# Performance work log

Hardware: AMD Instinct MI355X
Metric: run time of the kernel (lower is better)

## Reference

```python
import jax, jax.numpy as jnp
import numpy as np


def setup_inputs() -> dict:
    key = jax.random.key(0)
    k1, k2, k3 = jax.random.split(key, 3)
    B, D, T, DEPTH = 16384, 512, 64, 6
    x = jax.random.normal(k1, (B, D), dtype=jnp.float32)
    # per-tree learned params, stacked over the tree axis (num_trees)
    feature_selectors = jax.random.normal(k2, (T, DEPTH, D), dtype=jnp.float32)
    thresholds = jnp.zeros((T, DEPTH), dtype=jnp.float32)
    leaf_weights = jax.random.normal(k3, (T, 2 ** DEPTH, 1), dtype=jnp.float32)
    return {"x": x, "feature_selectors": feature_selectors,
            "thresholds": thresholds, "leaf_weights": leaf_weights}


def reference(x, feature_selectors, thresholds, leaf_weights):
    # x: [B, D]; feature_selectors: [T, depth, D]; thresholds: [T, depth]
    # leaf_weights: [T, 2^depth, 1]
    B = x.shape[0]
    T, depth, _ = feature_selectors.shape
    # all trees' split logits in one GEMM: [B, T, depth]
    logits = jnp.einsum('bi,tdi->btd', x, feature_selectors) - thresholds
    probs = jax.nn.sigmoid(logits)
    # probs_stack[..., 0] = p, probs_stack[..., 1] = 1 - p  -> [B, T, depth, 2]
    probs_stack = jnp.stack([probs, 1.0 - probs], axis=-1)
    # build leaf probabilities via repeated outer products over the depth axis
    leaf = probs_stack[:, :, 0]  # [B, T, 2]
    for d in range(1, depth):
        # [B, T, 2^d, 1] * [B, T, 1, 2] -> [B, T, 2^(d+1)]
        leaf = (leaf[..., :, None] * probs_stack[:, :, d][:, :, None, :]).reshape(B, T, -1)
    # per-tree leaf_probs @ weights, summed over trees -> [B, 1]
    out = jnp.einsum('btl,tlo->bo', leaf, leaf_weights)
    return out
```

## Files before the change

kernel.cpp:

```cpp
#include <hip/hip_runtime.h>


#define DD     512
#define NCOL   384
#define NDEPTH 6

typedef __bf16 bf16_t;
typedef __bf16 bf16x8 __attribute__((ext_vector_type(8)));
typedef float  f32x4  __attribute__((ext_vector_type(4)));

static __device__ __forceinline__ float b2f(unsigned int u16) {
  unsigned int t = u16 << 16;
  float f;
  __builtin_memcpy(&f, &t, 4);
  return f;
}

__global__ __launch_bounds__(256) void node_pack(const float* __restrict__ fsel,
                                                 bf16_t* __restrict__ pk)
{
  int tid  = blockIdx.x * 256 + threadIdx.x;
  int lane = tid & 63;
  int ksg  = (tid >> 6) & 15;
  int cf   = tid >> 10;
  int col  = cf * 16 + (lane & 15);
  int k    = ksg * 32 + (lane >> 4) * 8;
  float4 f0 = *reinterpret_cast<const float4*>(fsel + (size_t)col * DD + k);
  float4 f1 = *reinterpret_cast<const float4*>(fsel + (size_t)col * DD + k + 4);
  bf16x8 v;
  v[0] = (bf16_t)f0.x; v[1] = (bf16_t)f0.y; v[2] = (bf16_t)f0.z; v[3] = (bf16_t)f0.w;
  v[4] = (bf16_t)f1.x; v[5] = (bf16_t)f1.y; v[6] = (bf16_t)f1.z; v[7] = (bf16_t)f1.w;
  *reinterpret_cast<bf16x8*>(pk + (size_t)tid * 8) = v;
}

__global__ __launch_bounds__(512, 2) void node_fused(
    const float*  __restrict__ x,
    const bf16_t* __restrict__ pk,
    const float*  __restrict__ thr,
    const float*  __restrict__ lw,
    float*        __restrict__ out)
{
  __shared__ bf16_t xf[8192];
  __shared__ bf16_t pr[64 * NCOL];

  const int tid  = threadIdx.x;
  const int lane = tid & 63;
  const int wv   = tid >> 6;
  const int rowblk = blockIdx.x * 64;
  const int srow = lane & 15;
  const int skg  = lane >> 4;

  bf16x8 breg[3][16];
  #pragma unroll
  for (int f = 0; f < 3; ++f) {
    #pragma unroll
    for (int ks = 0; ks < 16; ++ks) {
      breg[f][ks] = *reinterpret_cast<const bf16x8*>(
          pk + ((size_t)(((wv * 3 + f) * 16 + ks) * 64) + lane) * 8);
    }
  }

  float th[3];
  #pragma unroll
  for (int f = 0; f < 3; ++f) th[f] = thr[wv * 48 + f * 16 + (lane & 15)];

  float4 st[4];

  #define ISSUE_LOADS(t)                                                        \
    do {                                                                        \
      const float* base_ = x + (size_t)(rowblk + (t) * 16 + srow) * DD + skg*8; \
      st[0] = *reinterpret_cast<const float4*>(base_ + wv * 32);                \
      st[1] = *reinterpret_cast<const float4*>(base_ + wv * 32 + 4);            \
      st[2] = *reinterpret_cast<const float4*>(base_ + (wv + 8) * 32);          \
      st[3] = *reinterpret_cast<const float4*>(base_ + (wv + 8) * 32 + 4);      \
    } while (0)

  #define WRITE_LDS()                                                           \
    do {                                                                        \
      bf16x8 v0_, v1_;                                                          \
      v0_[0]=(bf16_t)st[0].x; v0_[1]=(bf16_t)st[0].y;                           \
      v0_[2]=(bf16_t)st[0].z; v0_[3]=(bf16_t)st[0].w;                           \
      v0_[4]=(bf16_t)st[1].x; v0_[5]=(bf16_t)st[1].y;                           \
      v0_[6]=(bf16_t)st[1].z; v0_[7]=(bf16_t)st[1].w;                           \
      v1_[0]=(bf16_t)st[2].x; v1_[1]=(bf16_t)st[2].y;                           \
      v1_[2]=(bf16_t)st[2].z; v1_[3]=(bf16_t)st[2].w;                           \
      v1_[4]=(bf16_t)st[3].x; v1_[5]=(bf16_t)st[3].y;                           \
      v1_[6]=(bf16_t)st[3].z; v1_[7]=(bf16_t)st[3].w;                           \
      *reinterpret_cast<bf16x8*>(&xf[(wv * 64 + lane) * 8])       = v0_;        \
      *reinterpret_cast<bf16x8*>(&xf[((wv + 8) * 64 + lane) * 8]) = v1_;        \
    } while (0)

  ISSUE_LOADS(0);

  #pragma unroll
  for (int t = 0; t < 4; ++t) {
    WRITE_LDS();
    if (t < 3) ISSUE_LOADS(t + 1);
    asm volatile("s_waitcnt lgkmcnt(0)" ::: "memory");
    __builtin_amdgcn_s_barrier();

    f32x4 acc[3];
    #pragma unroll
    for (int f = 0; f < 3; ++f) acc[f] = (f32x4){0.f, 0.f, 0.f, 0.f};

    #pragma unroll
    for (int ks = 0; ks < 16; ++ks) {
      bf16x8 a = *reinterpret_cast<const bf16x8*>(&xf[(ks * 64 + lane) * 8]);
      acc[0] = __builtin_amdgcn_mfma_f32_16x16x32_bf16(a, breg[0][ks], acc[0], 0, 0, 0);
      acc[1] = __builtin_amdgcn_mfma_f32_16x16x32_bf16(a, breg[1][ks], acc[1], 0, 0, 0);
      acc[2] = __builtin_amdgcn_mfma_f32_16x16x32_bf16(a, breg[2][ks], acc[2], 0, 0, 0);
    }

    #pragma unroll
    for (int f = 0; f < 3; ++f) {
      const int col = wv * 48 + f * 16 + (lane & 15);
      #pragma unroll
      for (int r = 0; r < 4; ++r) {
        const int row = t * 16 + (lane >> 4) * 4 + r;
        float z = acc[f][r] - th[f];
        float p = 1.0f / (1.0f + __expf(-z));
        pr[row * NCOL + col] = (bf16_t)p;
      }
    }

    asm volatile("s_waitcnt lgkmcnt(0)" ::: "memory");
    __builtin_amdgcn_s_barrier();
  }
  #undef ISSUE_LOADS
  #undef WRITE_LDS

  float w[64];
  #pragma unroll
  for (int j = 0; j < 16; ++j) {
    float4 f = *reinterpret_cast<const float4*>(lw + (size_t)lane * 64 + j * 4);
    w[4*j] = f.x; w[4*j+1] = f.y; w[4*j+2] = f.z; w[4*j+3] = f.w;
  }

  #pragma unroll
  for (int rr = 0; rr < 8; ++rr) {
    const int row = wv * 8 + rr;
    const unsigned int* prow =
        reinterpret_cast<const unsigned int*>(pr + row * NCOL) + lane * 3;
    unsigned int d0 = prow[0], d1 = prow[1], d2 = prow[2];
    float p[NDEPTH];
    p[0] = b2f(d0 & 0xffffu); p[1] = b2f(d0 >> 16);
    p[2] = b2f(d1 & 0xffffu); p[3] = b2f(d1 >> 16);
    p[4] = b2f(d2 & 0xffffu); p[5] = b2f(d2 >> 16);

    float v[32];
    #pragma unroll
    for (int j = 0; j < 32; ++j) v[j] = fmaf(p[5], w[2*j] - w[2*j+1], w[2*j+1]);
    #pragma unroll
    for (int j = 0; j < 16; ++j) v[j] = fmaf(p[4], v[2*j] - v[2*j+1], v[2*j+1]);
    #pragma unroll
    for (int j = 0; j < 8;  ++j) v[j] = fmaf(p[3], v[2*j] - v[2*j+1], v[2*j+1]);
    #pragma unroll
    for (int j = 0; j < 4;  ++j) v[j] = fmaf(p[2], v[2*j] - v[2*j+1], v[2*j+1]);
    #pragma unroll
    for (int j = 0; j < 2;  ++j) v[j] = fmaf(p[1], v[2*j] - v[2*j+1], v[2*j+1]);
    float tv = fmaf(p[0], v[0] - v[1], v[1]);

    #pragma unroll
    for (int off = 32; off; off >>= 1) tv += __shfl_xor(tv, off, 64);
    if (lane == 0) out[rowblk + row] = tv;
  }
}

extern "C" void kernel_launch(void* const* d_in, const int* in_sizes, int n_in,
                              void* d_out, int out_size, void* d_ws, size_t ws_size,
                              hipStream_t stream) {
  const float* x    = (const float*)d_in[0];
  const float* fsel = (const float*)d_in[1];
  const float* thr  = (const float*)d_in[2];
  const float* lw   = (const float*)d_in[3];
  float* out = (float*)d_out;

  bf16_t* pk = (bf16_t*)d_ws;

  const int B = in_sizes[0] / DD;

  node_pack<<<dim3(96), dim3(256), 0, stream>>>(fsel, pk);
  node_fused<<<dim3(B / 64), dim3(512), 0, stream>>>(x, pk, thr, lw, out);
}
```

Measured before the change: 31.56 us.

## Replicate packed weights, pad LDS stride, batch reductions, pin register loads

The pack kernel now writes eight copies of the bf16 weight tile, and each block reads the copy chosen by its block index modulo 8. This spreads the heavy per-block weight loads over more cache lines and channels. The probability matrix in LDS is padded to a 392-element row stride to cut bank conflicts, and LDS moves to dynamic allocation. The per-row cross-lane reductions are batched into one shuffle pass across eight rows with unroll 2, and asm barriers keep the weight loads in registers. In exchange the pack kernel writes eight times as much data and register pressure rises.

```diff
diff --git a/kernel.cpp b/kernel.cpp
--- a/kernel.cpp
+++ b/kernel.cpp
@@ -4,6 +4,8 @@
 #define DD     512
 #define NCOL   384
 #define NDEPTH 6
+#define PKELT  (NCOL * DD)
+#define PRSTR  392
 
 typedef __bf16 bf16_t;
 typedef __bf16 bf16x8 __attribute__((ext_vector_type(8)));
@@ -30,18 +32,21 @@
   bf16x8 v;
   v[0] = (bf16_t)f0.x; v[1] = (bf16_t)f0.y; v[2] = (bf16_t)f0.z; v[3] = (bf16_t)f0.w;
   v[4] = (bf16_t)f1.x; v[5] = (bf16_t)f1.y; v[6] = (bf16_t)f1.z; v[7] = (bf16_t)f1.w;
-  *reinterpret_cast<bf16x8*>(pk + (size_t)tid * 8) = v;
+  #pragma unroll
+  for (int c = 0; c < 8; ++c)
+    *reinterpret_cast<bf16x8*>(pk + (size_t)c * PKELT + (size_t)tid * 8) = v;
 }
 
-__global__ __launch_bounds__(512, 2) void node_fused(
-    const float*  __restrict__ x,
-    const bf16_t* __restrict__ pk,
-    const float*  __restrict__ thr,
-    const float*  __restrict__ lw,
-    float*        __restrict__ out)
+__global__ void __launch_bounds__(512) __attribute__((amdgpu_waves_per_eu(2, 2)))
+node_fused(const float*  __restrict__ x,
+           const bf16_t* __restrict__ pk,
+           const float*  __restrict__ thr,
+           const float*  __restrict__ lw,
+           float*        __restrict__ out)
 {
-  __shared__ bf16_t xf[8192];
-  __shared__ bf16_t pr[64 * NCOL];
+  extern __shared__ char smem[];
+  bf16_t* xf = (bf16_t*)smem;
+  bf16_t* pr = (bf16_t*)(smem + 16384);
 
   const int tid  = threadIdx.x;
   const int lane = tid & 63;
@@ -49,6 +54,7 @@
   const int rowblk = blockIdx.x * 64;
   const int srow = lane & 15;
   const int skg  = lane >> 4;
+  const bf16_t* pkc = pk + (size_t)(blockIdx.x & 7) * PKELT;
 
   bf16x8 breg[3][16];
   #pragma unroll
@@ -56,7 +62,8 @@
     #pragma unroll
     for (int ks = 0; ks < 16; ++ks) {
       breg[f][ks] = *reinterpret_cast<const bf16x8*>(
-          pk + ((size_t)(((wv * 3 + f) * 16 + ks) * 64) + lane) * 8);
+          pkc + ((size_t)(((wv * 3 + f) * 16 + ks) * 64) + lane) * 8);
+      asm volatile("" : "+v"(breg[f][ks]));
     }
   }
 
@@ -119,7 +126,7 @@
         const int row = t * 16 + (lane >> 4) * 4 + r;
         float z = acc[f][r] - th[f];
         float p = 1.0f / (1.0f + __expf(-z));
-        pr[row * NCOL + col] = (bf16_t)p;
+        pr[row * PRSTR + col] = (bf16_t)p;
       }
     }
 
@@ -136,11 +143,12 @@
     w[4*j] = f.x; w[4*j+1] = f.y; w[4*j+2] = f.z; w[4*j+3] = f.w;
   }
 
-  #pragma unroll
+  float tvv[8];
+  #pragma unroll 2
   for (int rr = 0; rr < 8; ++rr) {
     const int row = wv * 8 + rr;
     const unsigned int* prow =
-        reinterpret_cast<const unsigned int*>(pr + row * NCOL) + lane * 3;
+        reinterpret_cast<const unsigned int*>(pr + row * PRSTR) + lane * 3;
     unsigned int d0 = prow[0], d1 = prow[1], d2 = prow[2];
     float p[NDEPTH];
     p[0] = b2f(d0 & 0xffffu); p[1] = b2f(d0 >> 16);
@@ -158,11 +166,17 @@
     for (int j = 0; j < 4;  ++j) v[j] = fmaf(p[2], v[2*j] - v[2*j+1], v[2*j+1]);
     #pragma unroll
     for (int j = 0; j < 2;  ++j) v[j] = fmaf(p[1], v[2*j] - v[2*j+1], v[2*j+1]);
-    float tv = fmaf(p[0], v[0] - v[1], v[1]);
+    tvv[rr] = fmaf(p[0], v[0] - v[1], v[1]);
+  }
 
+  #pragma unroll
+  for (int off = 32; off; off >>= 1) {
     #pragma unroll
-    for (int off = 32; off; off >>= 1) tv += __shfl_xor(tv, off, 64);
-    if (lane == 0) out[rowblk + row] = tv;
+    for (int rr = 0; rr < 8; ++rr) tvv[rr] += __shfl_xor(tvv[rr], off, 64);
+  }
+  if (lane == 0) {
+    #pragma unroll
+    for (int rr = 0; rr < 8; ++rr) out[rowblk + wv * 8 + rr] = tvv[rr];
   }
 }
 
@@ -178,7 +192,8 @@
   bf16_t* pk = (bf16_t*)d_ws;
 
   const int B = in_sizes[0] / DD;
+  const int lds = 16384 + 64 * PRSTR * 2;
 
   node_pack<<<dim3(96), dim3(256), 0, stream>>>(fsel, pk);
-  node_fused<<<dim3(B / 64), dim3(512), 0, stream>>>(x, pk, thr, lw, out);
+  node_fused<<<dim3(B / 64), dim3(512), lds, stream>>>(x, pk, thr, lw, out);
 }
```

After: 39.36 us. 1.25x slower.
